# Kernel tuning notes

Hardware: AMD Instinct MI355X
Metric: run time of the kernel (lower is better)

The kernel has to match this reference:

```python
import jax, jax.numpy as jnp
import numpy as np


def setup_inputs() -> dict:
    key = jax.random.key(0)
    ks = jax.random.split(key, 32)
    B, S, H, E, Vs, T = 32, 400, 512, 300, 200, 32
    EN, V = 50000, 50200
    rn = lambda k, shape, s=0.05: jax.random.normal(k, shape, jnp.float32) * s
    return {
        'encoder_hidden': rn(ks[0], (B, S, 2 * H), 1.0),
        'hidden0': rn(ks[1], (B, H), 1.0),
        'user_embed': rn(ks[2], (B, E), 1.0),
        'W_embed': rn(ks[3], (EN, E), 1.0),
        'W_ih': rn(ks[4], (3 * H, E)), 'W_hh': rn(ks[5], (3 * H, H)),
        'b_ih': rn(ks[6], (3 * H,)), 'b_hh': rn(ks[7], (3 * H,)),
        'Wk_c': rn(ks[8], (2 * H, H)), 'bk_c': rn(ks[9], (H,)),
        'Wq_c': rn(ks[10], (H, H)), 'bq_c': rn(ks[11], (H,)),
        'we_c': rn(ks[12], (H,)), 'be_c': rn(ks[13], (1,)),
        'Wk_u': rn(ks[14], (E, H)), 'bk_u': rn(ks[15], (H,)),
        'Wq_u': rn(ks[16], (H, H)), 'bq_u': rn(ks[17], (H,)),
        'we_u': rn(ks[18], (H,)), 'be_u': rn(ks[19], (1,)),
        'Wc': rn(ks[20], (3 * H + 2 * E, H)),
        'Wg': rn(ks[21], (3 * H + E,)), 'bg': rn(ks[22], (1,)),
        'Wgen': rn(ks[23], (H, EN)),
        'src_mask': jnp.ones((B, S), jnp.int32),
        'tgt_': jax.random.randint(ks[24], (B, T), 0, EN),
        'specific_vocab': jax.random.randint(ks[25], (B, Vs), 0, EN),
        'vocab_size': V,
    }


def reference(encoder_hidden, hidden0, user_embed, W_embed, W_ih, W_hh, b_ih, b_hh,
              Wk_c, bk_c, Wq_c, bq_c, we_c, be_c, Wk_u, bk_u, Wq_u, bq_u, we_u, be_u,
              Wc, Wg, bg, Wgen, src_mask, tgt_, specific_vocab, vocab_size):
    B, T = tgt_.shape
    # teacher forcing: prev token embed, step 0 uses <s> token id 1
    tgt_embed = W_embed[tgt_]                                  # [B,T,E]
    init_embed = jnp.broadcast_to(W_embed[1], (B, 1, W_embed.shape[1]))
    prev = jnp.concatenate([init_embed, tgt_embed[:, :T - 1]], axis=1)
    xs = jnp.swapaxes(prev, 0, 1)                              # [T,B,E]

    user_vocab_emb = W_embed[specific_vocab]                   # [B,Vs,E]
    proj_key_c = encoder_hidden @ Wk_c + bk_c                  # [B,S,H]
    proj_key_u = user_vocab_emb @ Wk_u + bk_u                  # [B,Vs,H]
    mask = src_mask != 0
    batch_idx = jnp.arange(B)[:, None]

    def gru_cell(h, x):
        gi = x @ W_ih.T + b_ih
        gh = h @ W_hh.T + b_hh
        i_r, i_z, i_n = jnp.split(gi, 3, axis=-1)
        h_r, h_z, h_n = jnp.split(gh, 3, axis=-1)
        r = jax.nn.sigmoid(i_r + h_r)
        z = jax.nn.sigmoid(i_z + h_z)
        n = jnp.tanh(i_n + r * h_n)
        return (1.0 - z) * n + z * h

    def step(h, x):
        h = gru_cell(h, x)                                     # [B,H]
        q = h
        # Bahdanau attention over encoder states
        sc = jnp.tanh((q @ Wq_c + bq_c)[:, None, :] + proj_key_c) @ we_c + be_c  # [B,S]
        sc = jnp.where(mask, sc, -1e9)
        ac = jax.nn.softmax(sc, axis=-1)
        ctx_c = jnp.einsum('bs,bsd->bd', ac, encoder_hidden)   # [B,2H]
        # Bahdanau attention over user-specific vocab embeddings
        su = jnp.tanh((q @ Wq_u + bq_u)[:, None, :] + proj_key_u) @ we_u + be_u  # [B,Vs]
        au = jax.nn.softmax(su, axis=-1)
        ctx_u = jnp.einsum('bv,bve->be', au, user_vocab_emb)   # [B,E]
        ch = jnp.tanh(jnp.concatenate([q, ctx_c, ctx_u, user_embed], axis=-1) @ Wc)
        gen_prob = jax.nn.softmax(ch @ Wgen, axis=-1)          # [B,embed_num]
        gen_prob = jnp.pad(gen_prob, ((0, 0), (0, vocab_size - gen_prob.shape[-1])))
        copy_prob = jnp.zeros((B, vocab_size), gen_prob.dtype).at[batch_idx, specific_vocab].add(au)
        copy_p = jax.nn.sigmoid(jnp.concatenate([ctx_c, q, ctx_u], axis=-1) @ Wg + bg[0])[:, None]
        mix = copy_p * copy_prob + (1.0 - copy_p) * gen_prob   # [B,vocab]
        return h, mix

    _, probs = jax.lax.scan(step, hidden0, xs)                 # [T,B,V]
    return jnp.swapaxes(probs, 0, 1)                           # [B,T,V]
```

## Files before the change

kernel.cpp:

```cpp
#include <hip/hip_runtime.h>


typedef __attribute__((ext_vector_type(8))) short short8;
typedef __attribute__((ext_vector_type(4))) float f32x4;
typedef unsigned short us;

#define SCW (-2.8853900817779268f)

__device__ __forceinline__ float bf2f(us u) {
  return __uint_as_float(((unsigned)u) << 16);
}
__device__ __forceinline__ us f2bf(float f) {
  unsigned x = __float_as_uint(f);
  unsigned r = x + 0x7fffu + ((x >> 16) & 1u);
  return (us)(r >> 16);
}
__device__ __forceinline__ float fsigmoid(float x) { return 1.f / (1.f + __expf(-x)); }
__device__ __forceinline__ float ftanh(float x) {
  float t = __expf(-2.f * fabsf(x));
  float r = (1.f - t) / (1.f + t);
  return x >= 0.f ? r : -r;
}
__device__ __forceinline__ float ftanh_fast(float x) {
  float u = exp2f(SCW * fabsf(x));
  float r = (1.f - u) * __builtin_amdgcn_rcpf(1.f + u);
  return copysignf(r, x);
}
__device__ __forceinline__ void unpack8(uint4 v, float* f) {
  f[0] = bf2f((us)(v.x & 0xffff)); f[1] = bf2f((us)(v.x >> 16));
  f[2] = bf2f((us)(v.y & 0xffff)); f[3] = bf2f((us)(v.y >> 16));
  f[4] = bf2f((us)(v.z & 0xffff)); f[5] = bf2f((us)(v.z >> 16));
  f[6] = bf2f((us)(v.w & 0xffff)); f[7] = bf2f((us)(v.w >> 16));
}

struct PP {
  const float *enc, *hidden0, *Wk_c, *Wk_u, *Wq_c, *Wq_u, *Wc, *W_ih, *W_hh, *W_embed;
  const int *tgt, *sv;
  us *encb, *hball, *WkcT, *WkuT, *WqcuT, *WcT, *WihT, *WhhF, *xe, *uve;
};

__device__ void tcast_job(const float* __restrict__ src, us* __restrict__ dst,
                          int R, int C, int Rpad, int x, int y, float scale,
                          int lt, float* tb) {
  int tx = lt & 31, ty = lt >> 5;
  int c0 = x * 32, r0 = y * 32;
#pragma unroll
  for (int i = 0; i < 4; ++i) {
    int r = r0 + ty + i * 8, c = c0 + tx;
    tb[(ty + i * 8) * 33 + tx] = (r < R && c < C) ? src[(size_t)r * C + c] : 0.f;
  }
  __syncthreads();
#pragma unroll
  for (int i = 0; i < 4; ++i) {
    int c = c0 + ty + i * 8, rr = r0 + tx;
    if (c < C && rr < Rpad)
      dst[(size_t)c * Rpad + rr] = f2bf(scale * tb[tx * 33 + ty + i * 8]);
  }
}

__global__ __launch_bounds__(256) void k_prep(PP P) {
  __shared__ float tb[32 * 33];
  const int bid = blockIdx.x, tid = threadIdx.x;
  if (bid < 1024) {
    for (int i = bid * 256 + tid; i < 3276800; i += 1024 * 256) {
      float4 v = ((const float4*)P.enc)[i];
      ushort4 o;
      o.x = f2bf(v.x); o.y = f2bf(v.y); o.z = f2bf(v.z); o.w = f2bf(v.w);
      ((ushort4*)P.encb)[i] = o;
    }
  } else if (bid < 1040) {
    int i = (bid - 1024) * 256 + tid;
    float4 v = ((const float4*)P.hidden0)[i];
    ushort4 o;
    o.x = f2bf(v.x); o.y = f2bf(v.y); o.z = f2bf(v.z); o.w = f2bf(v.w);
    ((ushort4*)P.hball)[i] = o;
  } else if (bid < 1552) {
    int j = bid - 1040;
    tcast_job(P.Wk_c, P.WkcT, 1024, 512, 1024, j & 15, j >> 4, SCW, tid, tb);
  } else if (bid < 1712) {
    int j = bid - 1552;
    tcast_job(P.Wk_u, P.WkuT, 300, 512, 320, j % 16, j / 16, SCW, tid, tb);
  } else if (bid < 1968) {
    int j = bid - 1712;
    tcast_job(P.Wq_c, P.WqcuT, 512, 512, 512, j & 15, j >> 4, SCW, tid, tb);
  } else if (bid < 2224) {
    int j = bid - 1968;
    tcast_job(P.Wq_u, P.WqcuT + 512ull * 512, 512, 512, 512, j & 15, j >> 4, SCW, tid, tb);
  } else if (bid < 3296) {
    int j = bid - 2224;
    tcast_job(P.Wc, P.WcT, 2136, 512, 2144, j % 16, j / 16, 1.f, tid, tb);
  } else if (bid < 3680) {
    int row = (bid - 3296) * 4 + (tid >> 6), k = tid & 63;
    for (int kk = k; kk < 320; kk += 64)
      P.WihT[(size_t)row * 320 + kk] =
          (kk < 300) ? f2bf(P.W_ih[(size_t)row * 300 + kk]) : (us)0;
  } else if (bid < 4064) {
    int job = (bid - 3680) * 4 + (tid >> 6), l = tid & 63;
    int q = job / 192, rem = job - q * 192, lt2 = rem >> 4, kt = rem & 15;
    int localrow = lt2 * 16 + (l & 15);
    int g = localrow >> 6, jj = localrow & 63;
    const float* src =
        P.W_hh + (size_t)(g * 512 + q * 64 + jj) * 512 + kt * 32 + (l >> 4) * 8;
    us* dst = P.WhhF + (((size_t)(q * 12 + lt2) * 16 + kt) * 64 + l) * 8;
#pragma unroll
    for (int i = 0; i < 8; ++i) dst[i] = f2bf(src[i]);
  } else if (bid < 4320) {
    int r = (bid - 4064) * 4 + (tid >> 6), k = tid & 63;
    int t = r >> 5, b = r & 31;
    int tok = (t == 0) ? 1 : P.tgt[b * 32 + (t - 1)];
    const float* src = P.W_embed + (size_t)tok * 300;
    for (int kk = k; kk < 320; kk += 64)
      P.xe[(size_t)r * 320 + kk] = (kk < 300) ? f2bf(src[kk]) : (us)0;
  } else {
    int row = (bid - 4320) * 4 + (tid >> 6), k = tid & 63;
    int tok = P.sv[row];
    const float* src = P.W_embed + (size_t)tok * 300;
    for (int kk = k; kk < 320; kk += 64)
      P.uve[(size_t)row * 320 + kk] = (kk < 300) ? f2bf(src[kk]) : (us)0;
  }
}

__global__ __launch_bounds__(256) void k_tcastX(const float* __restrict__ src0,
                                                us* __restrict__ dst0,
                                                int R, int C, int Rpad,
                                                size_t srcB, size_t dstB) {
  __shared__ float tile[32 * 33];
  const float* src = src0 + (size_t)blockIdx.z * srcB;
  us* dst = dst0 + (size_t)blockIdx.z * dstB;
  tcast_job(src, dst, R, C, Rpad, blockIdx.x, blockIdx.y, 1.f, threadIdx.x, tile);
}
__global__ __launch_bounds__(256) void k_tcastXb(const us* __restrict__ src0,
                                                 us* __restrict__ dst0,
                                                 int R, int C, int Rpad,
                                                 size_t srcB, size_t dstB) {
  __shared__ us tile[32][33];
  const us* src = src0 + (size_t)blockIdx.z * srcB;
  us* dst = dst0 + (size_t)blockIdx.z * dstB;
  int c0 = blockIdx.x * 32, r0 = blockIdx.y * 32;
  int tx = threadIdx.x & 31, ty = threadIdx.x >> 5;
#pragma unroll
  for (int i = 0; i < 4; ++i) {
    int r = r0 + ty + i * 8, c = c0 + tx;
    tile[ty + i * 8][tx] = (r < R && c < C) ? src[(size_t)r * C + c] : (us)0;
  }
  __syncthreads();
#pragma unroll
  for (int i = 0; i < 4; ++i) {
    int c = c0 + ty + i * 8, rr = r0 + tx;
    if (c < C && rr < Rpad) dst[(size_t)c * Rpad + rr] = tile[tx][ty + i * 8];
  }
}

template <int MODE, bool NM = false>
__global__ __launch_bounds__(512) void gemm_bt(const us* __restrict__ A,
                                               const us* __restrict__ BT,
                                               int M, int N, int K, int Ntiles,
                                               const float* __restrict__ bias,
                                               float bscale,
                                               us* __restrict__ outB,
                                               float* __restrict__ outF,
                                               float* __restrict__ rowsum) {
  __shared__ us sh[12288];
  __shared__ float rs[256];
  us* As = sh;
  us* Bs = sh + 8192;
  const int tid = threadIdx.x;
  const int lane = tid & 63, wid = tid >> 6;
  const int wr = wid >> 1, wc = wid & 1;
  const int bx = blockIdx.x;
  int mt, nt;
  if (NM) { mt = bx & 3; nt = bx >> 2; }
  else { mt = bx / Ntiles; nt = bx - mt * Ntiles; }
  const int m0 = mt * 256, n0 = nt * 128;
  f32x4 acc[4][4] = {};
  for (int kk = 0; kk < K; kk += 32) {
    uint4 av0, av1, bv;
    {
      int c = tid, row = c >> 2, c8 = (c & 3) * 8;
      av0 = *(const uint4*)(A + (size_t)(m0 + row) * K + kk + c8);
      c = tid + 512; row = c >> 2; c8 = (c & 3) * 8;
      av1 = *(const uint4*)(A + (size_t)(m0 + row) * K + kk + c8);
      c = tid; row = c >> 2; c8 = (c & 3) * 8;
      int nr = n0 + row; if (nr > N - 1) nr = N - 1;
      bv = *(const uint4*)(BT + (size_t)nr * K + kk + c8);
    }
    __syncthreads();
    ((uint4*)As)[tid] = av0;
    ((uint4*)As)[tid + 512] = av1;
    ((uint4*)Bs)[tid] = bv;
    __syncthreads();
    short8 af[4], bfr[4];
#pragma unroll
    for (int m = 0; m < 4; ++m)
      af[m] = *(const short8*)(As + (wr * 64 + m * 16 + (lane & 15)) * 32 + (lane >> 4) * 8);
#pragma unroll
    for (int n = 0; n < 4; ++n)
      bfr[n] = *(const short8*)(Bs + (wc * 64 + n * 16 + (lane & 15)) * 32 + (lane >> 4) * 8);
#pragma unroll
    for (int m = 0; m < 4; ++m)
#pragma unroll
      for (int n = 0; n < 4; ++n)
        acc[m][n] = __builtin_amdgcn_mfma_f32_16x16x32_bf16(af[m], bfr[n], acc[m][n], 0, 0, 0);
  }
  if (MODE == 0) {
#pragma unroll
    for (int m = 0; m < 4; ++m)
#pragma unroll
      for (int n = 0; n < 4; ++n)
#pragma unroll
        for (int reg = 0; reg < 4; ++reg) {
          int r = m0 + wr * 64 + m * 16 + (lane >> 4) * 4 + reg;
          int c = n0 + wc * 64 + n * 16 + (lane & 15);
          outB[(size_t)r * N + c] = f2bf(acc[m][n][reg] + bscale * bias[c]);
        }
  } else {
    if (tid < 256) rs[tid] = 0.f;
    __syncthreads();
#pragma unroll
    for (int m = 0; m < 4; ++m) {
#pragma unroll
      for (int reg = 0; reg < 4; ++reg) {
        int rloc = wr * 64 + m * 16 + (lane >> 4) * 4 + reg;
        float s = 0.f;
#pragma unroll
        for (int n = 0; n < 4; ++n) {
          int c = n0 + wc * 64 + n * 16 + (lane & 15);
          float e = (c < N) ? __expf(acc[m][n][reg]) : 0.f;
          if (MODE == 3) {
            int lrow = wr * 16 + (lane >> 4) * 4 + reg;
            int lcol = wc * 64 + n * 16 + (lane & 15);
            sh[lrow * 136 + lcol] = f2bf(e);
          } else if (c < N) {
            int r = m0 + rloc;
            size_t obase = (size_t)((r & 31) * 32 + (r >> 5)) * 50200;
            outF[obase + c] = e;
          }
          s += e;
        }
        s += __shfl_xor(s, 1, 64); s += __shfl_xor(s, 2, 64);
        s += __shfl_xor(s, 4, 64); s += __shfl_xor(s, 8, 64);
        if ((lane & 15) == 0) atomicAdd(&rs[rloc], s);
      }
      if (MODE == 3) {
        __syncthreads();
#pragma unroll
        for (int k2 = 0; k2 < 2; ++k2) {
          int idx = tid + k2 * 512;
          int l = idx >> 4, u = idx & 15;
          int r = m0 + (l >> 4) * 64 + m * 16 + (l & 15);
          size_t obase = (size_t)((r & 31) * 32 + (r >> 5)) * 50200;
          *(uint4*)(outB + obase + n0 + u * 8) = *(const uint4*)(sh + l * 136 + u * 8);
        }
        __syncthreads();
      }
    }
    __syncthreads();
    if (tid < 256) atomicAdd(&rowsum[m0 + tid], rs[tid]);
  }
}

template <int MODE>
__global__ __launch_bounds__(256) void gemm_med(const us* __restrict__ A,
                                                const us* __restrict__ BT,
                                                int M, int N, int K, int Ntiles,
                                                const float* __restrict__ bias,
                                                float bscale,
                                                us* __restrict__ outB) {
  __shared__ us As[64 * 32];
  __shared__ us Bs[128 * 32];
  const int tid = threadIdx.x, lane = tid & 63, w = tid >> 6;
  const int bx = blockIdx.x;
  const int mt = bx / Ntiles, nt = bx - mt * Ntiles;
  const int m0 = mt * 64, n0 = nt * 128;
  f32x4 acc[4][2] = {};
  for (int kk = 0; kk < K; kk += 32) {
    uint4 av, bv0, bv1;
    av = *(const uint4*)(A + (size_t)(m0 + (tid >> 2)) * K + kk + (tid & 3) * 8);
    {
      int i0 = tid * 2, i1 = tid * 2 + 1;
      bv0 = *(const uint4*)(BT + (size_t)(n0 + (i0 >> 2)) * K + kk + (i0 & 3) * 8);
      bv1 = *(const uint4*)(BT + (size_t)(n0 + (i1 >> 2)) * K + kk + (i1 & 3) * 8);
    }
    __syncthreads();
    ((uint4*)As)[tid] = av;
    ((uint4*)Bs)[tid * 2] = bv0;
    ((uint4*)Bs)[tid * 2 + 1] = bv1;
    __syncthreads();
    short8 af[4], bf0, bf1;
#pragma unroll
    for (int m = 0; m < 4; ++m)
      af[m] = *(const short8*)(As + (m * 16 + (lane & 15)) * 32 + (lane >> 4) * 8);
    bf0 = *(const short8*)(Bs + ((w * 2 + 0) * 16 + (lane & 15)) * 32 + (lane >> 4) * 8);
    bf1 = *(const short8*)(Bs + ((w * 2 + 1) * 16 + (lane & 15)) * 32 + (lane >> 4) * 8);
#pragma unroll
    for (int m = 0; m < 4; ++m) {
      acc[m][0] = __builtin_amdgcn_mfma_f32_16x16x32_bf16(af[m], bf0, acc[m][0], 0, 0, 0);
      acc[m][1] = __builtin_amdgcn_mfma_f32_16x16x32_bf16(af[m], bf1, acc[m][1], 0, 0, 0);
    }
  }
#pragma unroll
  for (int m = 0; m < 4; ++m)
#pragma unroll
    for (int q = 0; q < 2; ++q)
#pragma unroll
      for (int reg = 0; reg < 4; ++reg) {
        int r = m0 + m * 16 + (lane >> 4) * 4 + reg;
        int c = n0 + (w * 2 + q) * 16 + (lane & 15);
        float v = acc[m][q][reg];
        if (MODE == 0) v += bscale * bias[c];
        else v = ftanh_fast(v);
        outB[(size_t)r * N + c] = f2bf(v);
      }
}

struct FP {
  const us* frag; const us* gib; const float* bhh; const float* hidden0;
  us* hball; int* arrive;
  const us* encb; const us* WkcT; const float* bkc; us* pkc;
  const us* uve; const us* WkuT; const float* bku; us* pku;
  const float* Wgen; us* WT;
  const float* enc; us* encTp;
  us* uveTp;
};

__device__ void gru_body(const FP& P, int q, int tid, char* pool) {
  us* hs = (us*)pool;
  float* gh = (float*)(pool + 32768);
  const int lane = tid & 63, w = tid >> 6;
  short8 bfr[16];
  {
    const us* fb = P.frag + (((size_t)(q * 12 + w) * 16) * 64 + lane) * 8;
#pragma unroll
    for (int kt = 0; kt < 16; ++kt) bfr[kt] = *(const short8*)(fb + (size_t)kt * 512);
  }
  float hprev[3];
#pragma unroll
  for (int s = 0; s < 3; ++s) {
    int i = tid + s * 768;
    if (i < 2048) {
      int b = i >> 6, jj = i & 63;
      hprev[s] = P.hidden0[b * 512 + q * 64 + jj];
    }
  }
  const int sw = (lane & 7) << 3;
  for (int t = 0; t < 32; ++t) {
    if (t > 0) {
      if (tid == 0) {
        while (__hip_atomic_load(P.arrive + (t - 1), __ATOMIC_ACQUIRE,
                                 __HIP_MEMORY_SCOPE_AGENT) < 8) {
          __builtin_amdgcn_s_sleep(1);
        }
      }
      __syncthreads();
    }
    const us* hp = P.hball + (size_t)t * 16384;
    for (int i = tid; i < 2048; i += 768)
      ((uint4*)hs)[i ^ ((i >> 6) & 7)] = *(const uint4*)(hp + i * 8);
    __syncthreads();
    f32x4 acc0 = {}, acc1 = {};
#pragma unroll
    for (int kt = 0; kt < 16; ++kt) {
      int base0 = ((lane & 15) * 512 + kt * 32 + (lane >> 4) * 8) ^ sw;
      int base1 = (((lane & 15) + 16) * 512 + kt * 32 + (lane >> 4) * 8) ^ sw;
      short8 a0 = *(const short8*)(hs + base0);
      short8 a1 = *(const short8*)(hs + base1);
      acc0 = __builtin_amdgcn_mfma_f32_16x16x32_bf16(a0, bfr[kt], acc0, 0, 0, 0);
      acc1 = __builtin_amdgcn_mfma_f32_16x16x32_bf16(a1, bfr[kt], acc1, 0, 0, 0);
    }
    {
      int col = w * 16 + (lane & 15);
#pragma unroll
      for (int reg = 0; reg < 4; ++reg) {
        gh[col * 33 + ((lane >> 4) * 4 + reg)] = acc0[reg];
        gh[col * 33 + (16 + (lane >> 4) * 4 + reg)] = acc1[reg];
      }
    }
    __syncthreads();
    us* hbn = P.hball + (size_t)(t + 1) * 16384;
#pragma unroll
    for (int s = 0; s < 3; ++s) {
      int i = tid + s * 768;
      if (i < 2048) {
        int b = i >> 6, jj = i & 63, j = q * 64 + jj;
        float g0 = gh[jj * 33 + b] + P.bhh[j];
        float g1 = gh[(64 + jj) * 33 + b] + P.bhh[512 + j];
        float g2 = gh[(128 + jj) * 33 + b] + P.bhh[1024 + j];
        size_t gbase = (size_t)(t * 32 + b) * 1536;
        float r_ = fsigmoid(bf2f(P.gib[gbase + j]) + g0);
        float z_ = fsigmoid(bf2f(P.gib[gbase + 512 + j]) + g1);
        float n_ = ftanh(bf2f(P.gib[gbase + 1024 + j]) + r_ * g2);
        float hv = (1.f - z_) * n_ + z_ * hprev[s];
        hprev[s] = hv;
        hbn[b * 512 + j] = f2bf(hv);
      }
    }
    __syncthreads();
    if (tid == 0)
      __hip_atomic_fetch_add(P.arrive + t, 1, __ATOMIC_RELEASE,
                             __HIP_MEMORY_SCOPE_AGENT);
  }
}

__device__ void gemm0_body(const us* A, const us* BT, int N, int K,
                           int mt, int nt, const float* bias, float bscale,
                           us* outB, int tid, char* pool) {
  us* As = (us*)pool;
  us* Bs = (us*)(pool + 16384);
  const bool act = tid < 512;
  const int lane = tid & 63, wid = (tid >> 6) & 7;
  const int wr = wid >> 1, wc = wid & 1;
  const int m0 = mt * 256, n0 = nt * 128;
  f32x4 acc[4][4] = {};
  for (int kk = 0; kk < K; kk += 32) {
    uint4 av0 = {0, 0, 0, 0}, av1 = {0, 0, 0, 0}, bv = {0, 0, 0, 0};
    if (act) {
      int c = tid, row = c >> 2, c8 = (c & 3) * 8;
      av0 = *(const uint4*)(A + (size_t)(m0 + row) * K + kk + c8);
      av1 = *(const uint4*)(A + (size_t)(m0 + 128 + row) * K + kk + c8);
      int nr = n0 + row; if (nr > N - 1) nr = N - 1;
      bv = *(const uint4*)(BT + (size_t)nr * K + kk + c8);
    }
    __syncthreads();
    if (act) {
      ((uint4*)As)[tid] = av0;
      ((uint4*)As)[tid + 512] = av1;
      ((uint4*)Bs)[tid] = bv;
    }
    __syncthreads();
    if (act) {
      short8 af[4], bfr[4];
#pragma unroll
      for (int m = 0; m < 4; ++m)
        af[m] = *(const short8*)(As + (wr * 64 + m * 16 + (lane & 15)) * 32 + (lane >> 4) * 8);
#pragma unroll
      for (int n = 0; n < 4; ++n)
        bfr[n] = *(const short8*)(Bs + (wc * 64 + n * 16 + (lane & 15)) * 32 + (lane >> 4) * 8);
#pragma unroll
      for (int m = 0; m < 4; ++m)
#pragma unroll
        for (int n = 0; n < 4; ++n)
          acc[m][n] = __builtin_amdgcn_mfma_f32_16x16x32_bf16(af[m], bfr[n], acc[m][n], 0, 0, 0);
    }
  }
  if (act) {
#pragma unroll
    for (int m = 0; m < 4; ++m)
#pragma unroll
      for (int n = 0; n < 4; ++n)
#pragma unroll
        for (int reg = 0; reg < 4; ++reg) {
          int r = m0 + wr * 64 + m * 16 + (lane >> 4) * 4 + reg;
          int c = n0 + wc * 64 + n * 16 + (lane & 15);
          outB[(size_t)r * N + c] = f2bf(acc[m][n][reg] + bscale * bias[c]);
        }
  }
}

__global__ __launch_bounds__(768, 1) void k_fat(FP P) {
  __shared__ char pool[58368];
  const int bid = blockIdx.x, tid = threadIdx.x;
  if (bid < 8) { gru_body(P, bid, tid, pool); return; }
  if (bid < 208) {
    int j = bid - 8;
    gemm0_body(P.encb, P.WkcT, 512, 1024, j >> 2, j & 3, P.bkc, SCW, P.pkc, tid, pool);
    return;
  }
  if (bid < 308) {
    int j = bid - 208;
    gemm0_body(P.uve, P.WkuT, 512, 320, j >> 2, j & 3, P.bku, SCW, P.pku, tid, pool);
    return;
  }
  const int g = tid >> 8, lt = tid & 255;
  const int tx = lt & 31, ty = lt >> 5;
  float* tb = (float*)(pool + g * 4224);
  if (bid < 830) {
    int base = (bid - 308) * 3 + g;
    for (int it = 0; it < 16; ++it) {
      int sub = base + it * 1566;
      bool valid = sub < 25008;
      int x = valid ? sub % 1563 : 0, y = valid ? sub / 1563 : 0;
      int c0 = x * 32, r0 = y * 32;
      if (valid) {
#pragma unroll
        for (int i = 0; i < 4; ++i) {
          int r = r0 + ty + i * 8, c = c0 + tx;
          tb[(ty + i * 8) * 33 + tx] =
              (c < 50000) ? P.Wgen[(size_t)r * 50000 + c] : 0.f;
        }
      }
      __syncthreads();
      if (valid) {
#pragma unroll
        for (int i = 0; i < 4; ++i) {
          int c = c0 + ty + i * 8;
          if (c < 50000)
            P.WT[(size_t)c * 512 + r0 + tx] = f2bf(tb[tx * 33 + ty + i * 8]);
        }
      }
      __syncthreads();
    }
    return;
  }
  if (bid < 1108) {
    int base = (bid - 830) * 3 + g;
    for (int it = 0; it < 16; ++it) {
      int sub = base + it * 834;
      bool valid = sub < 13312;
      int x = sub & 31, rem = sub >> 5;
      int y = rem % 13, z = rem / 13;
      const float* src = P.enc + (size_t)z * 409600;
      us* dst = P.encTp + (size_t)z * 425984;
      int c0 = x * 32, r0 = y * 32;
      if (valid) {
#pragma unroll
        for (int i = 0; i < 4; ++i) {
          int r = r0 + ty + i * 8, c = c0 + tx;
          tb[(ty + i * 8) * 33 + tx] = (r < 400) ? src[(size_t)r * 1024 + c] : 0.f;
        }
      }
      __syncthreads();
      if (valid) {
#pragma unroll
        for (int i = 0; i < 4; ++i) {
          int c = c0 + ty + i * 8, rr = r0 + tx;
          if (rr < 416) dst[(size_t)c * 416 + rr] = f2bf(tb[tx * 33 + ty + i * 8]);
        }
      }
      __syncthreads();
    }
    return;
  }
  {
    us* tbu = (us*)tb;
    int base = (bid - 1108) * 3 + g;
    for (int it = 0; it < 16; ++it) {
      int sub = base + it * 141;
      bool valid = sub < 2240;
      int x = sub % 10, rem = sub / 10;
      int y = rem % 7, z = rem / 7;
      const us* src = P.uve + (size_t)z * 64000;
      us* dst = P.uveTp + (size_t)z * 71680;
      int c0 = x * 32, r0 = y * 32;
      if (valid) {
#pragma unroll
        for (int i = 0; i < 4; ++i) {
          int r = r0 + ty + i * 8, c = c0 + tx;
          tbu[(ty + i * 8) * 33 + tx] = (r < 200) ? src[(size_t)r * 320 + c] : (us)0;
        }
      }
      __syncthreads();
      if (valid) {
#pragma unroll
        for (int i = 0; i < 4; ++i) {
          int c = c0 + ty + i * 8, rr = r0 + tx;
          if (rr < 224) dst[(size_t)c * 224 + rr] = tbu[tx * 33 + ty + i * 8];
        }
      }
      __syncthreads();
    }
  }
}

__global__ __launch_bounds__(256) void k_scores(const us* __restrict__ Qall,
                                                const us* __restrict__ pkc,
                                                const us* __restrict__ pku,
                                                const float* __restrict__ wec,
                                                const float* __restrict__ bec,
                                                const float* __restrict__ weu,
                                                const float* __restrict__ beu,
                                                const int* __restrict__ src_mask,
                                                float* __restrict__ sc_enc,
                                                float* __restrict__ sc_usr) {
  __shared__ us q[16 * 512];
  const int bid = blockIdx.x;
  const bool enc = bid < 1600;
  int b, s0, th, qoff, S;
  if (enc) {
    b = bid / 50;
    int r = bid % 50;
    s0 = (r >> 1) * 16; th = r & 1; qoff = 0; S = 400;
  } else {
    int j = bid - 1600;
    b = j / 26;
    int r = j % 26;
    s0 = (r >> 1) * 16; th = r & 1; qoff = 512; S = 200;
  }
  for (int i = threadIdx.x; i < 1024; i += 256) {
    int tt = th * 16 + (i >> 6), c8 = (i & 63) * 8;
    ((uint4*)q)[i] = *(const uint4*)(Qall + (size_t)(tt * 32 + b) * 1024 + qoff + c8);
  }
  const int w = threadIdx.x >> 6, lane = threadIdx.x & 63;
  const int d0 = lane * 8;
  const float* we = enc ? wec : weu;
  float wef[8];
  {
    float4 w0 = *(const float4*)(we + d0);
    float4 w1 = *(const float4*)(we + d0 + 4);
    wef[0] = w0.x; wef[1] = w0.y; wef[2] = w0.z; wef[3] = w0.w;
    wef[4] = w1.x; wef[5] = w1.y; wef[6] = w1.z; wef[7] = w1.w;
  }
  const float bias = enc ? bec[0] : beu[0];
  float pkf[4][8];
  int ss[4], validv[4], maskedv[4];
#pragma unroll
  for (int si = 0; si < 4; ++si) {
    int s = s0 + w * 4 + si;
    validv[si] = (s < S);
    int sc = validv[si] ? s : (S - 1);
    ss[si] = sc;
    const us* pk = enc ? pkc + ((size_t)b * 400 + sc) * 512
                       : pku + ((size_t)b * 200 + sc) * 512;
    unpack8(*(const uint4*)(pk + d0), pkf[si]);
    maskedv[si] = enc ? (src_mask[b * 400 + sc] == 0) : 0;
  }
  __syncthreads();
  for (int tl = 0; tl < 16; ++tl) {
    short8 qv = *(const short8*)(q + tl * 512 + d0);
    float qf[8];
#pragma unroll
    for (int d = 0; d < 8; ++d) qf[d] = bf2f((us)qv[d]);
#pragma unroll
    for (int si = 0; si < 4; ++si) {
      float a = 0.f;
#pragma unroll
      for (int d = 0; d < 8; ++d) {
        float x = qf[d] + pkf[si][d];
        float u = exp2f(-fabsf(x));
        float r2v = (1.f - u) * __builtin_amdgcn_rcpf(1.f + u);
        a = fmaf(copysignf(r2v, -x), wef[d], a);
      }
#pragma unroll
      for (int m = 1; m < 64; m <<= 1) a += __shfl_xor(a, m, 64);
      if (lane == 0 && validv[si]) {
        int t = th * 16 + tl;
        float v = a + bias;
        if (enc) sc_enc[(size_t)(t * 32 + b) * 400 + ss[si]] = maskedv[si] ? -1e9f : v;
        else sc_usr[(size_t)(t * 32 + b) * 200 + ss[si]] = v;
      }
    }
  }
}

__device__ __forceinline__ float bmax256(float v, float* r4, int tid) {
#pragma unroll
  for (int m = 1; m < 64; m <<= 1) v = fmaxf(v, __shfl_xor(v, m, 64));
  if ((tid & 63) == 0) r4[tid >> 6] = v;
  __syncthreads();
  float x = fmaxf(fmaxf(r4[0], r4[1]), fmaxf(r4[2], r4[3]));
  __syncthreads();
  return x;
}
__device__ __forceinline__ float bsum256(float v, float* r4, int tid) {
#pragma unroll
  for (int m = 1; m < 64; m <<= 1) v += __shfl_xor(v, m, 64);
  if ((tid & 63) == 0) r4[tid >> 6] = v;
  __syncthreads();
  float x = r4[0] + r4[1] + r4[2] + r4[3];
  __syncthreads();
  return x;
}

__global__ __launch_bounds__(256) void k_soft2(const float* __restrict__ sc_enc,
                                               const float* __restrict__ sc_usr,
                                               us* __restrict__ AC,
                                               us* __restrict__ AU,
                                               float* __restrict__ aual,
                                               float* __restrict__ cp_acc,
                                               const us* __restrict__ hball,
                                               const float* __restrict__ ue,
                                               const float* __restrict__ Wg,
                                               us* __restrict__ catall) {
  __shared__ float r4[4];
  int bid = blockIdx.x, tid = threadIdx.x;
  if (bid < 1024) {
    int t = bid >> 5, b = bid & 31;
    float v0 = (tid < 400) ? sc_enc[(size_t)bid * 400 + tid] : -3e38f;
    float v1 = (tid + 256 < 400) ? sc_enc[(size_t)bid * 400 + tid + 256] : -3e38f;
    float mx = bmax256(fmaxf(v0, v1), r4, tid);
    float e0 = (tid < 400) ? __expf(v0 - mx) : 0.f;
    float e1 = (tid + 256 < 400) ? __expf(v1 - mx) : 0.f;
    float inv = 1.f / bsum256(e0 + e1, r4, tid);
    us* ACb = AC + (size_t)(b * 32 + t) * 416;
    if (tid < 400) ACb[tid] = f2bf(e0 * inv);
    int s2 = tid + 256;
    if (s2 < 400) ACb[s2] = f2bf(e1 * inv);
    else if (s2 < 416) ACb[s2] = 0;
  } else if (bid < 2048) {
    int rr = bid - 1024;
    int t = rr >> 5, b = rr & 31;
    float v0 = (tid < 200) ? sc_usr[(size_t)rr * 200 + tid] : -3e38f;
    float mx = bmax256(v0, r4, tid);
    float e0 = (tid < 200) ? __expf(v0 - mx) : 0.f;
    float inv = 1.f / bsum256(e0, r4, tid);
    us* AUb = AU + (size_t)(b * 32 + t) * 224;
    if (tid < 200) {
      float a = e0 * inv;
      AUb[tid] = f2bf(a);
      aual[(size_t)rr * 200 + tid] = a;
    } else if (tid < 224) {
      AUb[tid] = 0;
    }
  } else if (bid < 2304) {
    int w = tid >> 6, lane = tid & 63;
    int row = (bid - 2048) * 4 + w;
    int t = row >> 5, b = row & 31;
    us* rowp = catall + (size_t)row * 2144;
    const us* hb = hball + (size_t)(t + 1) * 16384 + b * 512;
    *(uint4*)(rowp + lane * 8) = *(const uint4*)(hb + lane * 8);
    for (int i = lane; i < 308; i += 64)
      rowp[1836 + i] = (i < 300) ? f2bf(ue[b * 300 + i]) : (us)0;
  } else {
    int w = tid >> 6, lane = tid & 63, d0 = lane * 8;
#pragma unroll
    for (int k = 0; k < 2; ++k) {
      int row = (bid - 2304) * 8 + w * 2 + k;
      int t = row >> 5, b = row & 31;
      float hv[8];
      unpack8(*(const uint4*)(hball + (size_t)(t + 1) * 16384 + b * 512 + d0), hv);
      float4 g0 = *(const float4*)(Wg + 1024 + d0);
      float4 g1 = *(const float4*)(Wg + 1024 + d0 + 4);
      float a = hv[0] * g0.x + hv[1] * g0.y + hv[2] * g0.z + hv[3] * g0.w +
                hv[4] * g1.x + hv[5] * g1.y + hv[6] * g1.z + hv[7] * g1.w;
#pragma unroll
      for (int m = 1; m < 64; m <<= 1) a += __shfl_xor(a, m, 64);
      if (lane == 0) atomicAdd(&cp_acc[row], a);
    }
  }
}

__device__ void ctx_core(const us* Ab, const us* Bb, const float* Wg,
                         us* catall, float* cp_acc, int b, int N, int Kp,
                         int n0, int catOff, int wgOff, int Nvalid, int tid,
                         us* As, us* Bs, float* gaccs) {
  const int lane = tid & 63, w = tid >> 6;
  if (tid < 32) gaccs[tid] = 0.f;
  f32x4 acc[2][2] = {};
  for (int kk = 0; kk < Kp; kk += 32) {
    uint4 av, bv0, bv1;
    if (tid < 128) av = *(const uint4*)(Ab + (size_t)(tid >> 2) * Kp + kk + (tid & 3) * 8);
    {
      int i0 = tid * 2, row0 = i0 >> 2, c0 = (i0 & 3) * 8;
      int i1 = tid * 2 + 1, row1 = i1 >> 2, c1 = (i1 & 3) * 8;
      int nr0 = n0 + row0; if (nr0 > N - 1) nr0 = N - 1;
      int nr1 = n0 + row1; if (nr1 > N - 1) nr1 = N - 1;
      bv0 = *(const uint4*)(Bb + (size_t)nr0 * Kp + kk + c0);
      bv1 = *(const uint4*)(Bb + (size_t)nr1 * Kp + kk + c1);
    }
    __syncthreads();
    if (tid < 128) ((uint4*)As)[tid] = av;
    ((uint4*)Bs)[tid * 2] = bv0;
    ((uint4*)Bs)[tid * 2 + 1] = bv1;
    __syncthreads();
    short8 a0 = *(const short8*)(As + ((lane & 15)) * 32 + (lane >> 4) * 8);
    short8 a1 = *(const short8*)(As + (16 + (lane & 15)) * 32 + (lane >> 4) * 8);
#pragma unroll
    for (int qq = 0; qq < 2; ++qq) {
      short8 bf_ = *(const short8*)(Bs + ((w * 2 + qq) * 16 + (lane & 15)) * 32 + (lane >> 4) * 8);
      acc[0][qq] = __builtin_amdgcn_mfma_f32_16x16x32_bf16(a0, bf_, acc[0][qq], 0, 0, 0);
      acc[1][qq] = __builtin_amdgcn_mfma_f32_16x16x32_bf16(a1, bf_, acc[1][qq], 0, 0, 0);
    }
  }
#pragma unroll
  for (int mt = 0; mt < 2; ++mt)
#pragma unroll
    for (int qq = 0; qq < 2; ++qq)
#pragma unroll
      for (int reg = 0; reg < 4; ++reg) {
        int t_ = mt * 16 + (lane >> 4) * 4 + reg;
        int c = n0 + (w * 2 + qq) * 16 + (lane & 15);
        if (c < Nvalid) {
          float v = acc[mt][qq][reg];
          catall[(size_t)(t_ * 32 + b) * 2144 + catOff + c] = f2bf(v);
          atomicAdd(&gaccs[t_], v * Wg[wgOff + c]);
        }
      }
  __syncthreads();
  if (tid < 32) atomicAdd(&cp_acc[tid * 32 + b], gaccs[tid]);
}

__global__ __launch_bounds__(256) void k_ctx2(const us* __restrict__ AC,
                                              const us* __restrict__ encTp,
                                              const us* __restrict__ AU,
                                              const us* __restrict__ uveTp,
                                              const float* __restrict__ Wg,
                                              us* __restrict__ catall,
                                              float* __restrict__ cp_acc) {
  __shared__ us As[32 * 32];
  __shared__ us Bs[128 * 32];
  __shared__ float gaccs[32];
  int bid = blockIdx.x, tid = threadIdx.x;
  if (bid < 256) {
    int b = bid >> 3, nt = bid & 7;
    ctx_core(AC + (size_t)b * 32 * 416, encTp + (size_t)b * 1024 * 416, Wg,
             catall, cp_acc, b, 1024, 416, nt * 128, 512, 0, 1024, tid, As, Bs, gaccs);
  } else {
    int j = bid - 256;
    int b = j / 3, nt = j % 3;
    ctx_core(AU + (size_t)b * 32 * 224, uveTp + (size_t)b * 320 * 224, Wg,
             catall, cp_acc, b, 320, 224, nt * 128, 1536, 1536, 300, tid, As, Bs, gaccs);
  }
}

__global__ __launch_bounds__(256) void k_finalize(float* __restrict__ out,
                                                  const float* __restrict__ rowsum,
                                                  const float* __restrict__ cp_acc,
                                                  const float* __restrict__ bg,
                                                  const float* __restrict__ au_all,
                                                  const int* __restrict__ sv) {
  int r = blockIdx.x, t = threadIdx.x;
  int b = r & 31, tt = r >> 5;
  float cp = fsigmoid(cp_acc[r] + bg[0]);
  float scale = (1.f - cp) / rowsum[r];
  float* base = out + (size_t)(b * 32 + tt) * 50200;
  float4* b4 = (float4*)base;
  for (int i = t; i < 12550; i += 256) {
    if (i < 12500) {
      float4 v = b4[i];
      v.x *= scale; v.y *= scale; v.z *= scale; v.w *= scale;
      b4[i] = v;
    } else {
      b4[i] = make_float4(0.f, 0.f, 0.f, 0.f);
    }
  }
  __syncthreads();
  if (t < 200) {
    int idx = sv[b * 200 + t];
    atomicAdd(base + idx, cp * au_all[(size_t)r * 200 + t]);
  }
}

__global__ __launch_bounds__(256) void k_finalize2(const us* __restrict__ expb,
                                                   const float* __restrict__ rowsum,
                                                   const float* __restrict__ cp_acc,
                                                   const float* __restrict__ bg,
                                                   const float* __restrict__ au_all,
                                                   const int* __restrict__ sv,
                                                   float* __restrict__ out) {
  int r = blockIdx.x, t = threadIdx.x;
  int b = r & 31, tt = r >> 5;
  float cp = fsigmoid(cp_acc[r] + bg[0]);
  float scale = (1.f - cp) / rowsum[r];
  size_t obase = (size_t)(b * 32 + tt) * 50200;
  const uint4* eb = (const uint4*)(expb + obase);
  float4* ob = (float4*)(out + obase);
  for (int i = t; i < 6275; i += 256) {
    float4 o0, o1;
    if (i < 6250) {
      uint4 ev = eb[i];
      o0.x = bf2f((us)(ev.x & 0xffff)) * scale; o0.y = bf2f((us)(ev.x >> 16)) * scale;
      o0.z = bf2f((us)(ev.y & 0xffff)) * scale; o0.w = bf2f((us)(ev.y >> 16)) * scale;
      o1.x = bf2f((us)(ev.z & 0xffff)) * scale; o1.y = bf2f((us)(ev.z >> 16)) * scale;
      o1.z = bf2f((us)(ev.w & 0xffff)) * scale; o1.w = bf2f((us)(ev.w >> 16)) * scale;
    } else {
      o0 = make_float4(0.f, 0.f, 0.f, 0.f);
      o1 = o0;
    }
    ob[i * 2] = o0;
    ob[i * 2 + 1] = o1;
  }
  __syncthreads();
  if (t < 200) {
    int idx = sv[b * 200 + t];
    atomicAdd(out + obase + idx, cp * au_all[(size_t)r * 200 + t]);
  }
}


extern "C" void kernel_launch(void* const* d_in, const int* in_sizes, int n_in,
                              void* d_out, int out_size, void* d_ws, size_t ws_size,
                              hipStream_t stream) {
  (void)in_sizes; (void)n_in; (void)out_size;
  const float* enc = (const float*)d_in[0];
  const float* hidden0 = (const float*)d_in[1];
  const float* user_embed = (const float*)d_in[2];
  const float* W_embed = (const float*)d_in[3];
  const float* W_ih = (const float*)d_in[4];
  const float* W_hh = (const float*)d_in[5];
  const float* b_ih = (const float*)d_in[6];
  const float* b_hh = (const float*)d_in[7];
  const float* Wk_c = (const float*)d_in[8];
  const float* bk_c = (const float*)d_in[9];
  const float* Wq_c = (const float*)d_in[10];
  const float* bq_c = (const float*)d_in[11];
  const float* we_c = (const float*)d_in[12];
  const float* be_c = (const float*)d_in[13];
  const float* Wk_u = (const float*)d_in[14];
  const float* bk_u = (const float*)d_in[15];
  const float* Wq_u = (const float*)d_in[16];
  const float* bq_u = (const float*)d_in[17];
  const float* we_u = (const float*)d_in[18];
  const float* be_u = (const float*)d_in[19];
  const float* Wc = (const float*)d_in[20];
  const float* Wg = (const float*)d_in[21];
  const float* bg = (const float*)d_in[22];
  const float* Wgen = (const float*)d_in[23];
  const int* src_mask = (const int*)d_in[24];
  const int* tgt = (const int*)d_in[25];
  const int* sv = (const int*)d_in[26];
  float* out = (float*)d_out;

  char* base = (char*)d_ws;
  size_t off = 0;
  auto take = [&](size_t bytes) {
    char* p = base + off;
    off += (bytes + 255) & ~(size_t)255;
    return p;
  };
  us* WT = (us*)take(50000ull * 512 * 2);
  char* R0 = take(32ull * 1024 * 416 * 2);
  us* encb = (us*)R0;
  char* RCD = take(12800ull * 512 * 2 + 6400ull * 512 * 2);
  us* pkc = (us*)RCD;
  us* pku = (us*)(RCD + 12800ull * 512 * 2);
  us* AC = (us*)RCD;
  us* AU = (us*)(RCD + 860160);
  float* aual = (float*)(RCD + 860160 + 458752);
  us* catall = (us*)(RCD + 860160 + 458752 + 819200);
  us* chb = (us*)(RCD + 860160 + 458752 + 819200 + 4390912);
  us* uve = (us*)take(6400ull * 320 * 2);
  us* uveTp = (us*)take(32ull * 320 * 224 * 2);
  char* RG = take(2700000);
  us* WkcT = (us*)RG;
  us* WihT = (us*)(RG + 1048576);
  us* xe = (us*)(RG + 1048576 + 983040);
  us* WkuT = (us*)take(512ull * 320 * 2);
  us* WqcuT = (us*)take(1024ull * 512 * 2);
  us* WcT = (us*)take(512ull * 2144 * 2);
  us* WhhF = (us*)take(1536ull * 512 * 2);
  us* gib = (us*)take(1024ull * 1536 * 2);
  us* hball = (us*)take(33ull * 16384 * 2);
  us* Qall = (us*)take(1024ull * 1024 * 2);
  float* sc_enc = (float*)take(1024ull * 400 * 4);
  float* sc_usr = (float*)take(1024ull * 200 * 4);
  float* bqcu = (float*)take(1024 * 4);
  float* cp_acc = (float*)take(1024 * 4);
  float* rsum = (float*)take(1024 * 4);
  int* arrive = (int*)take(32 * 4);
  size_t expb_bytes = 1024ull * 50200 * 2;
  bool big_ws = (ws_size >= off + expb_bytes + 256);
  us* expb = big_ws ? (us*)take(expb_bytes) : nullptr;
  us* encTp = big_ws ? expb : (us*)R0;

  hipMemcpyAsync(bqcu, bq_c, 512 * 4, hipMemcpyDeviceToDevice, stream);
  hipMemcpyAsync(bqcu + 512, bq_u, 512 * 4, hipMemcpyDeviceToDevice, stream);
  hipMemsetAsync(rsum, 0, 1024 * 4, stream);
  hipMemsetAsync(cp_acc, 0, 1024 * 4, stream);
  hipMemsetAsync(arrive, 0, 32 * 4, stream);

  PP pp;
  pp.enc = enc; pp.hidden0 = hidden0; pp.Wk_c = Wk_c; pp.Wk_u = Wk_u;
  pp.Wq_c = Wq_c; pp.Wq_u = Wq_u; pp.Wc = Wc; pp.W_ih = W_ih; pp.W_hh = W_hh;
  pp.W_embed = W_embed; pp.tgt = tgt; pp.sv = sv;
  pp.encb = encb; pp.hball = hball; pp.WkcT = WkcT; pp.WkuT = WkuT;
  pp.WqcuT = WqcuT; pp.WcT = WcT; pp.WihT = WihT; pp.WhhF = WhhF;
  pp.xe = xe; pp.uve = uve;
  k_prep<<<5920, 256, 0, stream>>>(pp);
  gemm_med<0><<<192, 256, 0, stream>>>(xe, WihT, 1024, 1536, 320, 12, b_ih, 1.f, gib);

  FP fp;
  fp.frag = WhhF; fp.gib = gib; fp.bhh = b_hh; fp.hidden0 = hidden0;
  fp.hball = hball; fp.arrive = arrive;
  fp.encb = encb; fp.WkcT = WkcT; fp.bkc = bk_c; fp.pkc = pkc;
  fp.uve = uve; fp.WkuT = WkuT; fp.bku = bk_u; fp.pku = pku;
  fp.Wgen = Wgen; fp.WT = WT; fp.enc = enc; fp.encTp = encTp; fp.uveTp = uveTp;

  if (big_ws) {
    k_fat<<<1155, 768, 0, stream>>>(fp);
  } else {
    k_tcastX<<<dim3(1563, 16, 1), 256, 0, stream>>>(Wgen, WT, 512, 50000, 512, 0, 0);
    gemm_bt<0><<<200, 512, 0, stream>>>(encb, WkcT, 12800, 512, 1024, 4, bk_c, SCW,
                                        pkc, nullptr, nullptr);
    gemm_bt<0><<<100, 512, 0, stream>>>(uve, WkuT, 6400, 512, 320, 4, bk_u, SCW,
                                        pku, nullptr, nullptr);
    k_tcastX<<<dim3(32, 13, 32), 256, 0, stream>>>(enc, encTp, 400, 1024, 416,
                                                   400ull * 1024, 1024ull * 416);
    k_tcastXb<<<dim3(10, 7, 32), 256, 0, stream>>>(uve, uveTp, 200, 320, 224,
                                                   200ull * 320, 320ull * 224);
    k_fat<<<8, 768, 0, stream>>>(fp);
  }

  gemm_med<0><<<128, 256, 0, stream>>>(hball + 16384, WqcuT, 1024, 1024, 512, 8,
                                       bqcu, SCW, Qall);
  k_scores<<<2432, 256, 0, stream>>>(Qall, pkc, pku, we_c, be_c, we_u, be_u,
                                     src_mask, sc_enc, sc_usr);
  k_soft2<<<2432, 256, 0, stream>>>(sc_enc, sc_usr, AC, AU, aual, cp_acc,
                                    hball, user_embed, Wg, catall);
  k_ctx2<<<352, 256, 0, stream>>>(AC, encTp, AU, uveTp, Wg, catall, cp_acc);
  gemm_med<2><<<64, 256, 0, stream>>>(catall, WcT, 1024, 512, 2144, 4, nullptr,
                                      1.f, chb);
  if (big_ws) {
    gemm_bt<3, true><<<4 * 391, 512, 0, stream>>>(chb, WT, 1024, 50000, 512, 391,
                                                  nullptr, 1.f, expb, nullptr, rsum);
    k_finalize2<<<1024, 256, 0, stream>>>(expb, rsum, cp_acc, bg, aual, sv, out);
  } else {
    gemm_bt<1, true><<<4 * 391, 512, 0, stream>>>(chb, WT, 1024, 50000, 512, 391,
                                                  nullptr, 1.f, nullptr, out, rsum);
    k_finalize<<<1024, 256, 0, stream>>>(out, rsum, cp_acc, bg, aual, sv);
  }
}
```

Baseline: 682.9 us.

## Add 256x256-tile exp GEMM kernel and hoist GRU bias/input-gate loads

Replaces the MODE 3 path of the large vocab-projection GEMM with a new 1024-thread kernel that uses 256x256 output tiles. Each A/B element is loaded once per K-slice for more output, reducing global traffic and block count (784 vs 1564). The exp'd bf16 results are staged through shared memory in four row groups to write coalesced rows. Separately, the GRU body hoists the b_hh loads out of the time loop and prefetches the input-gate values before the inter-block spin wait, so those loads overlap the barrier. The new kernel runs with 1 block per CU, few waves and no double buffering, so latency hiding may suffer.

```diff
diff --git a/kernel.cpp b/kernel.cpp
--- a/kernel.cpp
+++ b/kernel.cpp
@@ -226,11 +226,7 @@
         for (int n = 0; n < 4; ++n) {
           int c = n0 + wc * 64 + n * 16 + (lane & 15);
           float e = (c < N) ? __expf(acc[m][n][reg]) : 0.f;
-          if (MODE == 3) {
-            int lrow = wr * 16 + (lane >> 4) * 4 + reg;
-            int lcol = wc * 64 + n * 16 + (lane & 15);
-            sh[lrow * 136 + lcol] = f2bf(e);
-          } else if (c < N) {
+          if (c < N) {
             int r = m0 + rloc;
             size_t obase = (size_t)((r & 31) * 32 + (r >> 5)) * 50200;
             outF[obase + c] = e;
@@ -241,22 +237,84 @@
         s += __shfl_xor(s, 4, 64); s += __shfl_xor(s, 8, 64);
         if ((lane & 15) == 0) atomicAdd(&rs[rloc], s);
       }
-      if (MODE == 3) {
-        __syncthreads();
-#pragma unroll
-        for (int k2 = 0; k2 < 2; ++k2) {
-          int idx = tid + k2 * 512;
-          int l = idx >> 4, u = idx & 15;
-          int r = m0 + (l >> 4) * 64 + m * 16 + (l & 15);
-          size_t obase = (size_t)((r & 31) * 32 + (r >> 5)) * 50200;
-          *(uint4*)(outB + obase + n0 + u * 8) = *(const uint4*)(sh + l * 136 + u * 8);
-        }
-        __syncthreads();
-      }
     }
     __syncthreads();
     if (tid < 256) atomicAdd(&rowsum[m0 + tid], rs[tid]);
   }
+}
+
+__global__ __launch_bounds__(1024, 1) void gemm_v(const us* __restrict__ A,
+                                                  const us* __restrict__ BT,
+                                                  us* __restrict__ outB,
+                                                  float* __restrict__ rowsum) {
+  __shared__ us shp[16384];
+  __shared__ float rs[256];
+  us* As = shp;
+  us* Bs = shp + 8192;
+  const int tid = threadIdx.x;
+  const int lane = tid & 63, wid = tid >> 6;
+  const int wr2 = wid >> 2, wc2 = wid & 3;
+  const int bx = blockIdx.x;
+  const int mt = bx & 3, nt = bx >> 2;
+  const int m0 = mt * 256, n0 = nt * 256;
+  const int N = 50000;
+  const int srow = tid >> 2, sc8 = (tid & 3) * 8;
+  int bnr = n0 + srow; if (bnr > N - 1) bnr = N - 1;
+  f32x4 acc[4][4] = {};
+  for (int kk = 0; kk < 512; kk += 32) {
+    uint4 av = *(const uint4*)(A + (size_t)(m0 + srow) * 512 + kk + sc8);
+    uint4 bv = *(const uint4*)(BT + (size_t)bnr * 512 + kk + sc8);
+    __syncthreads();
+    ((uint4*)As)[tid] = av;
+    ((uint4*)Bs)[tid] = bv;
+    __syncthreads();
+    short8 af[4], bfr[4];
+#pragma unroll
+    for (int m = 0; m < 4; ++m)
+      af[m] = *(const short8*)(As + (wr2 * 64 + m * 16 + (lane & 15)) * 32 + (lane >> 4) * 8);
+#pragma unroll
+    for (int n = 0; n < 4; ++n)
+      bfr[n] = *(const short8*)(Bs + (wc2 * 64 + n * 16 + (lane & 15)) * 32 + (lane >> 4) * 8);
+#pragma unroll
+    for (int m = 0; m < 4; ++m)
+#pragma unroll
+      for (int n = 0; n < 4; ++n)
+        acc[m][n] = __builtin_amdgcn_mfma_f32_16x16x32_bf16(af[m], bfr[n], acc[m][n], 0, 0, 0);
+  }
+  if (tid < 256) rs[tid] = 0.f;
+  __syncthreads();
+  for (int g = 0; g < 4; ++g) {
+    if (wr2 == g) {
+#pragma unroll
+      for (int m = 0; m < 4; ++m)
+#pragma unroll
+        for (int reg = 0; reg < 4; ++reg) {
+          int rloc_g = m * 16 + (lane >> 4) * 4 + reg;
+          float s = 0.f;
+#pragma unroll
+          for (int n = 0; n < 4; ++n) {
+            int c = n0 + wc2 * 64 + n * 16 + (lane & 15);
+            float e = (c < N) ? __expf(acc[m][n][reg]) : 0.f;
+            shp[rloc_g * 256 + wc2 * 64 + n * 16 + (lane & 15)] = f2bf(e);
+            s += e;
+          }
+          s += __shfl_xor(s, 1, 64); s += __shfl_xor(s, 2, 64);
+          s += __shfl_xor(s, 4, 64); s += __shfl_xor(s, 8, 64);
+          if ((lane & 15) == 0) atomicAdd(&rs[g * 64 + rloc_g], s);
+        }
+    }
+    __syncthreads();
+#pragma unroll
+    for (int k2 = 0; k2 < 2; ++k2) {
+      int idx = tid + k2 * 1024;
+      int l = idx >> 5, u = idx & 31;
+      int r = m0 + g * 64 + l;
+      size_t obase = (size_t)((r & 31) * 32 + (r >> 5)) * 50200;
+      *(uint4*)(outB + obase + n0 + u * 8) = *(const uint4*)(shp + l * 256 + u * 8);
+    }
+    __syncthreads();
+  }
+  if (tid < 256) atomicAdd(&rowsum[m0 + tid], rs[tid]);
 }
 
 template <int MODE>
@@ -333,17 +391,30 @@
 #pragma unroll
     for (int kt = 0; kt < 16; ++kt) bfr[kt] = *(const short8*)(fb + (size_t)kt * 512);
   }
-  float hprev[3];
+  float hprev[3], bh0[3], bh1[3], bh2[3];
 #pragma unroll
   for (int s = 0; s < 3; ++s) {
     int i = tid + s * 768;
     if (i < 2048) {
-      int b = i >> 6, jj = i & 63;
-      hprev[s] = P.hidden0[b * 512 + q * 64 + jj];
+      int b = i >> 6, jj = i & 63, j = q * 64 + jj;
+      hprev[s] = P.hidden0[b * 512 + j];
+      bh0[s] = P.bhh[j]; bh1[s] = P.bhh[512 + j]; bh2[s] = P.bhh[1024 + j];
     }
   }
   const int sw = (lane & 7) << 3;
   for (int t = 0; t < 32; ++t) {
+    float gi0[3], gi1[3], gi2[3];
+#pragma unroll
+    for (int s = 0; s < 3; ++s) {
+      int i = tid + s * 768;
+      if (i < 2048) {
+        int b = i >> 6, jj = i & 63, j = q * 64 + jj;
+        size_t gbase = (size_t)(t * 32 + b) * 1536;
+        gi0[s] = bf2f(P.gib[gbase + j]);
+        gi1[s] = bf2f(P.gib[gbase + 512 + j]);
+        gi2[s] = bf2f(P.gib[gbase + 1024 + j]);
+      }
+    }
     if (t > 0) {
       if (tid == 0) {
         while (__hip_atomic_load(P.arrive + (t - 1), __ATOMIC_ACQUIRE,
@@ -382,13 +453,12 @@
       int i = tid + s * 768;
       if (i < 2048) {
         int b = i >> 6, jj = i & 63, j = q * 64 + jj;
-        float g0 = gh[jj * 33 + b] + P.bhh[j];
-        float g1 = gh[(64 + jj) * 33 + b] + P.bhh[512 + j];
-        float g2 = gh[(128 + jj) * 33 + b] + P.bhh[1024 + j];
-        size_t gbase = (size_t)(t * 32 + b) * 1536;
-        float r_ = fsigmoid(bf2f(P.gib[gbase + j]) + g0);
-        float z_ = fsigmoid(bf2f(P.gib[gbase + 512 + j]) + g1);
-        float n_ = ftanh(bf2f(P.gib[gbase + 1024 + j]) + r_ * g2);
+        float g0 = gh[jj * 33 + b] + bh0[s];
+        float g1 = gh[(64 + jj) * 33 + b] + bh1[s];
+        float g2 = gh[(128 + jj) * 33 + b] + bh2[s];
+        float r_ = fsigmoid(gi0[s] + g0);
+        float z_ = fsigmoid(gi1[s] + g1);
+        float n_ = ftanh(gi2[s] + r_ * g2);
         float hv = (1.f - z_) * n_ + z_ * hprev[s];
         hprev[s] = hv;
         hbn[b * 512 + j] = f2bf(hv);
@@ -989,8 +1059,7 @@
   gemm_med<2><<<64, 256, 0, stream>>>(catall, WcT, 1024, 512, 2144, 4, nullptr,
                                       1.f, chb);
   if (big_ws) {
-    gemm_bt<3, true><<<4 * 391, 512, 0, stream>>>(chb, WT, 1024, 50000, 512, 391,
-                                                  nullptr, 1.f, expb, nullptr, rsum);
+    gemm_v<<<784, 1024, 0, stream>>>(chb, WT, expb, rsum);
     k_finalize2<<<1024, 256, 0, stream>>>(expb, rsum, cp_acc, bg, aual, sv, out);
   } else {
     gemm_bt<1, true><<<4 * 391, 512, 0, stream>>>(chb, WT, 1024, 50000, 512, 391,
```

Measured after the change: 705.3 us. 1.03x slower.
